# Kernel optimization log

Hardware: AMD Instinct MI355X
Metric: run time of the kernel (lower is better)

The kernel has to match this reference:

```python
import jax, jax.numpy as jnp
import numpy as np

MAX_TRAV = 21  # matches the torch module constant


def setup_inputs() -> dict:
    key = jax.random.key(0)
    k1, _ = jax.random.split(key)
    B, H, W = 4, 2048, 2048
    untraversable = jax.random.randint(k1, (B, H, W), 0, 2).astype(jnp.bool_)
    max_sq = jnp.ones((1,), dtype=jnp.float32) * float(MAX_TRAV ** 2)  # 441.0
    return {"untraversable": untraversable, "max_sq": max_sq}


def _chamfer(untraversable, max_sq):
    big = max_sq[0]
    B, H, W = untraversable.shape
    # 0 at obstacles, MAX_TRAV^2 elsewhere (values are small exact ints in fp32)
    sq = jnp.where(untraversable, jnp.float32(0.0), big)
    # odd increments 1,3,...,41: cumulative sum of first k odds = k^2
    ds = jnp.arange(1, 2 * MAX_TRAV + 1, 2, dtype=jnp.float32)

    col = jnp.full((B, H, 1), big, dtype=jnp.float32)

    def hstep(s, d):
        from_right = jnp.concatenate([s[:, :, 1:] + d, col], axis=2)
        from_left = jnp.concatenate([col, s[:, :, :-1] + d], axis=2)
        return jnp.minimum(s, jnp.minimum(from_right, from_left)), None

    sq, _ = jax.lax.scan(hstep, sq, ds)

    row = jnp.full((B, 1, W), big, dtype=jnp.float32)

    def vstep(s, d):
        from_below = jnp.concatenate([s[:, 1:, :] + d, row], axis=1)
        from_above = jnp.concatenate([row, s[:, :-1, :] + d], axis=1)
        return jnp.minimum(s, jnp.minimum(from_below, from_above)), None

    sq, _ = jax.lax.scan(vstep, sq, ds)
    return jnp.sqrt(sq)


def reference(untraversable, max_sq):
    return _chamfer(untraversable, max_sq)
```

## Files before the change

### kernel.cpp

```cpp
#include <hip/hip_runtime.h>
#include <cstdint>

#define BB 4
#define HH 2048
#define WW 2048
#define MAXT 21
#define BIGSQ 441

static __device__ __forceinline__ uint32_t umin32(uint32_t a, uint32_t b) { return a < b ? a : b; }

__global__ __launch_bounds__(256) void hpass(const int* __restrict__ in,
                                             uint8_t* __restrict__ dh) {
    const int tid  = threadIdx.x;
    const int lane = tid & 63;
    const int w    = tid >> 6;
    const int row  = blockIdx.x;
    const long long ro = (long long)row * WW;
    const int x0   = w << 9;

    int v[8];
    #pragma unroll
    for (int j = 0; j < 8; ++j)
        v[j] = in[ro + x0 + (j << 6) + lane];

    unsigned long long b[10];
    b[0] = 0; b[9] = 0;
    if (x0 > 0)
        b[0] = __ballot(in[ro + x0 - 64 + lane] != 0);
    if (x0 + 512 < WW)
        b[9] = __ballot(in[ro + x0 + 512 + lane] != 0);
    #pragma unroll
    for (int j = 0; j < 8; ++j)
        b[j + 1] = __ballot(v[j] != 0);

    #pragma unroll
    for (int j = 0; j < 8; ++j) {
        const unsigned long long mc = b[j + 1];
        unsigned long long right = mc >> lane;
        if (lane) right |= b[j + 2] << (64 - lane);
        unsigned long long left = mc << (63 - lane);
        if (lane != 63) left |= b[j] >> (lane + 1);

        int dr = right ? __builtin_ctzll(right) : 64;
        int dl = left  ? __builtin_clzll(left)  : 64;
        int d  = min(min(dr, dl), MAXT);
        dh[ro + x0 + (j << 6) + lane] = (uint8_t)d;
    }
}

__global__ __launch_bounds__(256) void vpass(const uint8_t* __restrict__ dh,
                                             float* __restrict__ out) {
    __shared__ uint16_t s[106][128];
    const int tid = threadIdx.x;
    const int x0  = blockIdx.x << 7;
    const int y0  = blockIdx.y << 6;
    const int b   = blockIdx.z;
    const long long base = (long long)b * HH * WW;

    for (int i = tid; i < 106 * 16; i += 256) {
        int r  = i >> 4;
        int c8 = (i & 15) << 3;
        int gy = y0 - 21 + r;
        uint4 pk;
        if (gy >= 0 && gy < HH) {
            const uint8_t* p = dh + base + (long long)gy * WW + x0 + c8;
            uint2 u = *(const uint2*)p;
            uint32_t e0 = u.x & 0xff, e1 = (u.x >> 8) & 0xff, e2 = (u.x >> 16) & 0xff, e3 = u.x >> 24;
            uint32_t e4 = u.y & 0xff, e5 = (u.y >> 8) & 0xff, e6 = (u.y >> 16) & 0xff, e7 = u.y >> 24;
            pk.x = (e0 * e0) | ((e1 * e1) << 16);
            pk.y = (e2 * e2) | ((e3 * e3) << 16);
            pk.z = (e4 * e4) | ((e5 * e5) << 16);
            pk.w = (e6 * e6) | ((e7 * e7) << 16);
        } else {
            pk.x = pk.y = pk.z = pk.w = BIGSQ | (BIGSQ << 16);
        }
        *(uint4*)&s[r][c8] = pk;
    }
    __syncthreads();

    const int lane = tid & 63;
    const int w    = tid >> 6;
    const int cg   = (lane & 31) << 2;
    const int ro   = lane >> 5;
    for (int k = 0; k < 8; ++k) {
        const int j  = (w << 4) + (k << 1) + ro;
        const int yl = 21 + j;

        uint2 q = *(const uint2*)&s[yl][cg];
        uint32_t v0 = q.x & 0xffff, v1 = q.x >> 16;
        uint32_t v2 = q.y & 0xffff, v3 = q.y >> 16;

        for (int d = 1; d <= MAXT; ++d) {
            const uint32_t dd = (uint32_t)(d * d);
            uint32_t h = umin32(0, 0);
            h = v0 > v1 ? v0 : v1;
            uint32_t h2 = v2 > v3 ? v2 : v3;
            h = h > h2 ? h : h2;
            if (__all(dd >= h)) break;
            uint2 a  = *(const uint2*)&s[yl - d][cg];
            uint2 bq = *(const uint2*)&s[yl + d][cg];
            const uint32_t dd2 = dd * 0x10001u;
            uint32_t A0 = a.x + dd2, A1 = a.y + dd2;
            uint32_t B0 = bq.x + dd2, B1 = bq.y + dd2;
            v0 = umin32(v0, umin32(A0 & 0xffff, B0 & 0xffff));
            v1 = umin32(v1, umin32(A0 >> 16,    B0 >> 16));
            v2 = umin32(v2, umin32(A1 & 0xffff, B1 & 0xffff));
            v3 = umin32(v3, umin32(A1 >> 16,    B1 >> 16));
        }

        float4 o;
        o.x = sqrtf((float)v0);
        o.y = sqrtf((float)v1);
        o.z = sqrtf((float)v2);
        o.w = sqrtf((float)v3);
        *(float4*)&out[base + (long long)(y0 + j) * WW + x0 + cg] = o;
    }
}

extern "C" void kernel_launch(void* const* d_in, const int* in_sizes, int n_in,
                              void* d_out, int out_size, void* d_ws, size_t ws_size,
                              hipStream_t stream) {
    const int* unt = (const int*)d_in[0];
    uint8_t* dh    = (uint8_t*)d_ws;
    float* out     = (float*)d_out;

    hpass<<<dim3(BB * HH), 256, 0, stream>>>(unt, dh);
    vpass<<<dim3(WW / 128, HH / 64, BB), 256, 0, stream>>>(dh, out);
}
```

Baseline: 41.46 us.

## Vectorize hpass loads with one-row-per-wave bitmask scans, swizzle vpass blocks, nontemporal stores

```diff
diff --git a/kernel.cpp b/kernel.cpp
--- a/kernel.cpp
+++ b/kernel.cpp
@@ -6,45 +6,80 @@
 #define WW 2048
 #define MAXT 21
 #define BIGSQ 441
+#define SEN (1u << 6)
+
+typedef float floatx4 __attribute__((ext_vector_type(4)));
 
 static __device__ __forceinline__ uint32_t umin32(uint32_t a, uint32_t b) { return a < b ? a : b; }
+static __device__ __forceinline__ int imin(int a, int b) { return a < b ? a : b; }
 
 __global__ __launch_bounds__(256) void hpass(const int* __restrict__ in,
                                              uint8_t* __restrict__ dh) {
     const int tid  = threadIdx.x;
     const int lane = tid & 63;
     const int w    = tid >> 6;
-    const int row  = blockIdx.x;
+    const int row  = (blockIdx.x << 2) + w;
     const long long ro = (long long)row * WW;
-    const int x0   = w << 9;
+    const int* rp = in + ro;
+    const int li = 63 - lane;
 
-    int v[8];
+    uint4 q[8];
     #pragma unroll
     for (int j = 0; j < 8; ++j)
-        v[j] = in[ro + x0 + (j << 6) + lane];
+        q[j] = *(const uint4*)(rp + (j << 8) + (lane << 2));
 
-    unsigned long long b[10];
-    b[0] = 0; b[9] = 0;
-    if (x0 > 0)
-        b[0] = __ballot(in[ro + x0 - 64 + lane] != 0);
-    if (x0 + 512 < WW)
-        b[9] = __ballot(in[ro + x0 + 512 + lane] != 0);
+    unsigned long long Bc[4], Bn[4], rbc[4], rbp[4];
     #pragma unroll
-    for (int j = 0; j < 8; ++j)
-        b[j + 1] = __ballot(v[j] != 0);
+    for (int k = 0; k < 4; ++k) rbp[k] = 0;
+    Bc[0] = __ballot(q[0].x != 0);
+    Bc[1] = __ballot(q[0].y != 0);
+    Bc[2] = __ballot(q[0].z != 0);
+    Bc[3] = __ballot(q[0].w != 0);
+    #pragma unroll
+    for (int k = 0; k < 4; ++k) rbc[k] = __brevll(Bc[k]);
 
     #pragma unroll
     for (int j = 0; j < 8; ++j) {
-        const unsigned long long mc = b[j + 1];
-        unsigned long long right = mc >> lane;
-        if (lane) right |= b[j + 2] << (64 - lane);
-        unsigned long long left = mc << (63 - lane);
-        if (lane != 63) left |= b[j] >> (lane + 1);
+        if (j < 7) {
+            Bn[0] = __ballot(q[j + 1].x != 0);
+            Bn[1] = __ballot(q[j + 1].y != 0);
+            Bn[2] = __ballot(q[j + 1].z != 0);
+            Bn[3] = __ballot(q[j + 1].w != 0);
+        } else {
+            Bn[0] = Bn[1] = Bn[2] = Bn[3] = 0;
+        }
 
-        int dr = right ? __builtin_ctzll(right) : 64;
-        int dl = left  ? __builtin_clzll(left)  : 64;
-        int d  = min(min(dr, dl), MAXT);
-        dh[ro + x0 + (j << 6) + lane] = (uint8_t)d;
+        int a[4], b[4], c[4], e[4];
+        #pragma unroll
+        for (int k = 0; k < 4; ++k) {
+            unsigned long long S  = (Bc[k] >> lane) | ((Bn[k] << 1) << li);
+            unsigned long long SL = (rbc[k] >> li)  | ((rbp[k] << 1) << lane);
+            uint32_t s  = (uint32_t)S;
+            uint32_t sl = (uint32_t)SL;
+            a[k] = 4 * __builtin_ctz(s | SEN) + k;
+            b[k] = 4 * __builtin_ctz((s >> 1) | SEN) + 4 + k;
+            c[k] = 4 * __builtin_ctz(sl | SEN) - k;
+            e[k] = 4 * __builtin_ctz((sl >> 1) | SEN) + 4 - k;
+        }
+        const int A3 = a[3], A2 = imin(a[2], A3), A1 = imin(a[1], A2), A0 = imin(a[0], A1);
+        const int B0 = b[0], B1 = imin(B0, b[1]), B2 = imin(B1, b[2]);
+        const int C0 = c[0], C1 = imin(C0, c[1]), C2 = imin(C1, c[2]), C3 = imin(C2, c[3]);
+        const int E3 = e[3], E2 = imin(e[2], E3), E1 = imin(e[1], E2);
+
+        int d0 = imin(imin(A0,           imin(C0, E1)    ), MAXT);
+        int d1 = imin(imin(imin(A1, B0) - 1, imin(C1, E2) + 1), MAXT);
+        int d2 = imin(imin(imin(A2, B1) - 2, imin(C2, E3) + 2), MAXT);
+        int d3 = imin(imin(imin(A3, B2) - 3, C3 + 3          ), MAXT);
+
+        uint32_t pk = (uint32_t)d0 | ((uint32_t)d1 << 8) | ((uint32_t)d2 << 16) | ((uint32_t)d3 << 24);
+        *(uint32_t*)(dh + ro + (j << 8) + (lane << 2)) = pk;
+
+        #pragma unroll
+        for (int k = 0; k < 4; ++k) {
+            rbp[k] = rbc[k];
+            Bc[k]  = Bn[k];
+            rbc[k] = __brevll(Bn[k]);
+        }
     }
 }
 
@@ -52,29 +87,37 @@
                                              float* __restrict__ out) {
     __shared__ uint16_t s[106][128];
     const int tid = threadIdx.x;
-    const int x0  = blockIdx.x << 7;
-    const int y0  = blockIdx.y << 6;
-    const int b   = blockIdx.z;
+    const int bid = blockIdx.x;
+    const int swz = (bid & 7) * 256 + (bid >> 3);
+    const int x0  = (swz & 15) << 7;
+    const int y0  = ((swz >> 4) & 31) << 6;
+    const int b   = swz >> 9;
     const long long base = (long long)b * HH * WW;
 
-    for (int i = tid; i < 106 * 16; i += 256) {
-        int r  = i >> 4;
-        int c8 = (i & 15) << 3;
-        int gy = y0 - 21 + r;
-        uint4 pk;
+    for (int i = tid; i < 106 * 8; i += 256) {
+        const int r   = i >> 3;
+        const int c16 = (i & 7) << 4;
+        const int gy  = y0 - 21 + r;
+        uint4 pk0, pk1;
         if (gy >= 0 && gy < HH) {
-            const uint8_t* p = dh + base + (long long)gy * WW + x0 + c8;
-            uint2 u = *(const uint2*)p;
-            uint32_t e0 = u.x & 0xff, e1 = (u.x >> 8) & 0xff, e2 = (u.x >> 16) & 0xff, e3 = u.x >> 24;
-            uint32_t e4 = u.y & 0xff, e5 = (u.y >> 8) & 0xff, e6 = (u.y >> 16) & 0xff, e7 = u.y >> 24;
-            pk.x = (e0 * e0) | ((e1 * e1) << 16);
-            pk.y = (e2 * e2) | ((e3 * e3) << 16);
-            pk.z = (e4 * e4) | ((e5 * e5) << 16);
-            pk.w = (e6 * e6) | ((e7 * e7) << 16);
+            const uint8_t* p = dh + base + (long long)gy * WW + x0 + c16;
+            uint4 u = *(const uint4*)p;
+            #pragma unroll
+            for (int h = 0; h < 4; ++h) {
+                uint32_t word = (&u.x)[h];
+                uint32_t e0 = word & 0xff, e1 = (word >> 8) & 0xff;
+                uint32_t e2 = (word >> 16) & 0xff, e3 = word >> 24;
+                uint32_t lo = (e0 * e0) | ((e1 * e1) << 16);
+                uint32_t hi = (e2 * e2) | ((e3 * e3) << 16);
+                if (h < 2) { (&pk0.x)[h * 2] = lo; (&pk0.x)[h * 2 + 1] = hi; }
+                else       { (&pk1.x)[(h - 2) * 2] = lo; (&pk1.x)[(h - 2) * 2 + 1] = hi; }
+            }
         } else {
-            pk.x = pk.y = pk.z = pk.w = BIGSQ | (BIGSQ << 16);
+            pk0.x = pk0.y = pk0.z = pk0.w = BIGSQ | (BIGSQ << 16);
+            pk1 = pk0;
         }
-        *(uint4*)&s[r][c8] = pk;
+        *(uint4*)&s[r][c16]     = pk0;
+        *(uint4*)&s[r][c16 + 8] = pk1;
     }
     __syncthreads();
 
@@ -92,8 +135,7 @@
 
         for (int d = 1; d <= MAXT; ++d) {
             const uint32_t dd = (uint32_t)(d * d);
-            uint32_t h = umin32(0, 0);
-            h = v0 > v1 ? v0 : v1;
+            uint32_t h  = v0 > v1 ? v0 : v1;
             uint32_t h2 = v2 > v3 ? v2 : v3;
             h = h > h2 ? h : h2;
             if (__all(dd >= h)) break;
@@ -108,12 +150,13 @@
             v3 = umin32(v3, umin32(A1 >> 16,    B1 >> 16));
         }
 
-        float4 o;
+        floatx4 o;
         o.x = sqrtf((float)v0);
         o.y = sqrtf((float)v1);
         o.z = sqrtf((float)v2);
         o.w = sqrtf((float)v3);
-        *(float4*)&out[base + (long long)(y0 + j) * WW + x0 + cg] = o;
+        floatx4* op = (floatx4*)&out[base + (long long)(y0 + j) * WW + x0 + cg];
+        __builtin_nontemporal_store(o, op);
     }
 }
 
@@ -124,6 +167,6 @@
     uint8_t* dh    = (uint8_t*)d_ws;
     float* out     = (float*)d_out;
 
-    hpass<<<dim3(BB * HH), 256, 0, stream>>>(unt, dh);
-    vpass<<<dim3(WW / 128, HH / 64, BB), 256, 0, stream>>>(dh, out);
+    hpass<<<dim3(BB * HH / 4), 256, 0, stream>>>(unt, dh);
+    vpass<<<dim3(WW / 128 * HH / 64 * BB), 256, 0, stream>>>(dh, out);
 }
```

New measurement: 37.99 us. -8.4%, faster.
